# Performance work log

Measured on AMD Instinct MI355X. Metric: run time of the kernel, lower is better.

Reference implementation:

```python
import jax, jax.numpy as jnp
import numpy as np

B = 4096
D = 68 * 68  # 4624
L = 68
E = 1024


def setup_inputs() -> dict:
    key = jax.random.key(0)
    ks = jax.random.split(key, 24)
    rn = lambda k, shape, scale: jax.random.normal(k, shape, dtype=jnp.float32) * scale
    inp = {
        "x": rn(ks[0], (B, D), 1.0),
        "eps": rn(ks[1], (B, L), 1.0),
        # weights scaled ~1/sqrt(fan_in) to avoid sigmoid saturation
        "fc11_w": rn(ks[2], (E, D), 1.0 / np.sqrt(D)),
        "fc11_b": rn(ks[3], (E,), 0.01),
        "fc12_w": rn(ks[4], (E, D), 1.0 / np.sqrt(D)),
        "fc12_b": rn(ks[5], (E,), 0.01),
        "fc21_w": rn(ks[6], (L, E), 1.0 / np.sqrt(E)),
        "fc21_b": rn(ks[7], (L,), 0.01),
        "fc22_w": rn(ks[8], (L, E), 1.0 / np.sqrt(E)),
        "fc22_b": rn(ks[9], (L,), 0.01),
        "W3": rn(ks[10], (5, L, L), 1.0 / np.sqrt(L)),
        "b3": rn(ks[11], (5, L), 0.01),
        "W4": rn(ks[12], (5, L, L), 1.0 / np.sqrt(L)),
        "b4": rn(ks[13], (5, L), 0.01),
        "W5": rn(ks[14], (3, L, L), 1.0 / np.sqrt(L)),
        "b5": rn(ks[15], (3, L), 0.01),
        "fc6_w": rn(ks[16], (D, D), 1.0 / np.sqrt(D)),
        "fc6_b": rn(ks[17], (D,), 0.01),
        "fcy_w": rn(ks[18], (1, L), 1.0 / np.sqrt(L)),
        "fcy_b": rn(ks[19], (1,), 0.01),
    }
    return inp


def _forward(x, eps, fc11_w, fc11_b, fc12_w, fc12_b, fc21_w, fc21_b,
             fc22_w, fc22_b, W3, b3, W4, b4, W5, b5, fc6_w, fc6_b, fcy_w, fcy_b):
    b = x.shape[0]
    # encode (dropout in eval mode -> identity)
    h11 = jax.nn.relu(x @ fc11_w.T + fc11_b)
    h12 = jax.nn.relu(x @ fc12_w.T + fc12_b)
    mu = h11 @ fc21_w.T + fc21_b          # [B, 68]
    logvar = h12 @ fc22_w.T + fc22_b      # [B, 68]
    # reparameterize
    z = mu + eps * jnp.exp(0.5 * logvar)
    y = mu @ fcy_w.T + fcy_b              # [B, 1]
    # decode: 5 parallel 68-dim branches (vectorized over branch axis k)
    h3 = jnp.einsum('bd,kod->kbo', z, W3) + b3[:, None, :]     # [5,B,68]
    # source: h31 has no sigmoid, h32..h35 do
    h3 = jnp.concatenate([h3[:1], jax.nn.sigmoid(h3[1:])], axis=0)
    h4 = jax.nn.sigmoid(jnp.einsum('kbd,kod->kbo', h3, W4) + b4[:, None, :])
    # source reuses fc53 for branches 4 and 5: weight index map [0,1,2,2,2]
    idx = jnp.array([0, 1, 2, 2, 2])
    h5 = jnp.einsum('kbd,kod->kbo', h4, W5[idx]) + b5[idx][:, None, :]  # [5,B,68]
    # source: h6 = h51 only (other branch outer-products are dead code)
    h51 = h5[0]                                                # [B,68]
    outer = (h51[:, :, None] * h51[:, None, :]).reshape(b, D)  # bmm outer product
    recon = jax.nn.sigmoid(outer @ fc6_w.T + fc6_b)            # [B, 4624]
    return recon, mu, logvar, y


def reference(x, eps, fc11_w, fc11_b, fc12_w, fc12_b, fc21_w, fc21_b,
              fc22_w, fc22_b, W3, b3, W4, b4, W5, b5, fc6_w, fc6_b, fcy_w, fcy_b):
    return _forward(x, eps, fc11_w, fc11_b, fc12_w, fc12_b, fc21_w, fc21_b,
                    fc22_w, fc22_b, W3, b3, W4, b4, W5, b5, fc6_w, fc6_b, fcy_w, fcy_b)
```

## Files before the change

### kernel.cpp

```cpp
#include <hip/hip_runtime.h>
#include <hip/hip_bf16.h>
#include <cstdint>
#include <cstddef>

typedef __bf16 bf16x8 __attribute__((ext_vector_type(8)));
typedef __bf16 bf16x4 __attribute__((ext_vector_type(4)));
typedef float  floatx4 __attribute__((ext_vector_type(4)));

#define DEV __device__ __forceinline__

DEV __bf16 f2b(float x) { return (__bf16)x; }

DEV void async_ld16(const void* g, void* l) {
    __builtin_amdgcn_global_load_lds(
        (const __attribute__((address_space(1))) unsigned int*)g,
        (__attribute__((address_space(3))) unsigned int*)l,
        16, 0, 0);
}

#define BATCH 4096
#define DDIM  4624
#define DPAD  4800
#define LDIM  68
#define EDIM  1024
#define N1    2048
#define KB    2048
#define N2PAD 4864
#define NPAIR 2346
#define K2PAD 2496

__global__ void cvt_pad(const float* __restrict__ src, int rows_valid, int K,
                        __bf16* __restrict__ dst, int rows_total) {
    const int gpr = DPAD / 4;
    const long total = (long)rows_total * gpr;
    for (long g = blockIdx.x * (long)blockDim.x + threadIdx.x; g < total;
         g += gridDim.x * (long)blockDim.x) {
        int row = (int)(g / gpr);
        int c4  = (int)(g - (long)row * gpr) * 4;
        bf16x4 v;
        if (row < rows_valid && c4 < K) {
            floatx4 f = *(const floatx4*)(src + (size_t)row * K + c4);
            v[0] = f2b(f[0]); v[1] = f2b(f[1]); v[2] = f2b(f[2]); v[3] = f2b(f[3]);
        } else {
            v[0] = v[1] = v[2] = v[3] = (__bf16)0.0f;
        }
        *(bf16x4*)(dst + (size_t)row * DPAD + c4) = v;
    }
}

__global__ void pad_w2(const float* __restrict__ w21, const float* __restrict__ w22,
                       __bf16* __restrict__ dst) {
    const int total = 144 * 512;
    for (int g = blockIdx.x * blockDim.x + threadIdx.x; g < total;
         g += gridDim.x * blockDim.x) {
        int row = g >> 9;
        int c4  = (g & 511) * 4;
        bf16x4 v;
        v[0] = v[1] = v[2] = v[3] = (__bf16)0.0f;
        if (row < 68 && c4 < 1024) {
            floatx4 f = *(const floatx4*)(w21 + (size_t)row * EDIM + c4);
            v[0] = f2b(f[0]); v[1] = f2b(f[1]); v[2] = f2b(f[2]); v[3] = f2b(f[3]);
        } else if (row >= 68 && row < 136 && c4 >= 1024) {
            floatx4 f = *(const floatx4*)(w22 + (size_t)(row - 68) * EDIM + (c4 - 1024));
            v[0] = f2b(f[0]); v[1] = f2b(f[1]); v[2] = f2b(f[2]); v[3] = f2b(f[3]);
        }
        *(bf16x4*)(dst + (size_t)row * KB + c4) = v;
    }
}

DEV void build_ptab(unsigned short* ptab, int t, int nthr) {
    for (int i = t; i < LDIM; i += nthr) {
        int p0 = i * (137 - i) / 2;
        for (int j = i; j < LDIM; ++j)
            ptab[p0 + (j - i)] = (unsigned short)((i << 8) | j);
    }
}

__global__ void w6sym_build(const float* __restrict__ w6, __bf16* __restrict__ dst) {
    __shared__ float row[DDIM];
    __shared__ unsigned short ptab[K2PAD];
    const int o = blockIdx.x;
    const int t = threadIdx.x;
    if (o < DDIM) {
        const float* src = w6 + (size_t)o * DDIM;
        for (int idx = t; idx < DDIM / 4; idx += 256)
            *(floatx4*)(row + idx * 4) = *(const floatx4*)(src + idx * 4);
    }
    build_ptab(ptab, t, 256);
    __syncthreads();
    for (int p4 = t; p4 < K2PAD / 4; p4 += 256) {
        bf16x4 v;
#pragma unroll
        for (int u = 0; u < 4; ++u) {
            int p = p4 * 4 + u;
            float val = 0.f;
            if (o < DDIM && p < NPAIR) {
                int ij = ptab[p];
                int i = ij >> 8, j = ij & 255;
                val = (i == j) ? row[i * LDIM + i] : (row[i * LDIM + j] + row[j * LDIM + i]);
            }
            v[u] = f2b(val);
        }
        *(bf16x4*)(dst + (size_t)o * K2PAD + p4 * 4) = v;
    }
}

template <int EPI>
__launch_bounds__(512, 1)
__global__ void gemm_bt(const __bf16* __restrict__ A, int lda,
                        const __bf16* __restrict__ W, int ldb, int KT,
                        __bf16* __restrict__ outb, float* __restrict__ outf, int ldc,
                        const float* __restrict__ bias0, const float* __restrict__ bias1) {
    __shared__ __align__(16) __bf16 smA[3 * 128 * 64];
    __shared__ __align__(16) __bf16 smB[3 * 256 * 64];

    const int t  = threadIdx.x;
    const int l  = t & 63;
    const int w  = t >> 6;
    const int m0 = blockIdx.x * 128;
    const int n0 = blockIdx.y * 256;
    const int wm = (w & 1) * 64;
    const int wn = (w >> 1) * 64;

    const int lr = t >> 3;
    const int sw = (t & 7) ^ (lr & 7);
    const __bf16* pa0 = A + (size_t)(m0 + lr) * lda + sw * 8;
    const __bf16* pb0 = W + (size_t)(n0 + lr) * ldb + sw * 8;
    char* dA = (char*)smA + t * 16;
    char* dB = (char*)smB + t * 16;

    const int q  = l >> 4;
    const int ra = wm + (l & 15);
    const int rb = wn + (l & 15);

    floatx4 acc[4][4];
#pragma unroll
    for (int mi = 0; mi < 4; ++mi)
#pragma unroll
        for (int ni = 0; ni < 4; ++ni) {
            floatx4 z = {0.f, 0.f, 0.f, 0.f};
            acc[mi][ni] = z;
        }

    auto STAGE = [&](int tile, int buf) {
        const __bf16* sa = pa0 + (size_t)tile * 64;
        const __bf16* sb = pb0 + (size_t)tile * 64;
        char* da = dA + buf * 16384;
        char* db = dB + buf * 32768;
        async_ld16(sa,                        da);
        async_ld16(sa + (size_t)64  * lda,    da + 8192);
        async_ld16(sb,                        db);
        async_ld16(sb + (size_t)64  * ldb,    db + 8192);
        async_ld16(sb + (size_t)128 * ldb,    db + 16384);
        async_ld16(sb + (size_t)192 * ldb,    db + 24576);
    };

    auto COMPUTE = [&](int ba, int bb) {
        const char* baseA = (const char*)smA + ba;
        const char* baseB = (const char*)smB + bb;
#pragma unroll
        for (int h = 0; h < 2; ++h) {
            const int c = ((h << 2) | q) ^ (l & 7);
            bf16x8 af[4], bfr[4];
#pragma unroll
            for (int mi = 0; mi < 4; ++mi)
                af[mi] = *(const bf16x8*)(baseA + (ra + mi * 16) * 128 + c * 16);
#pragma unroll
            for (int ni = 0; ni < 4; ++ni)
                bfr[ni] = *(const bf16x8*)(baseB + (rb + ni * 16) * 128 + c * 16);
            __builtin_amdgcn_s_setprio(1);
#pragma unroll
            for (int mi = 0; mi < 4; ++mi)
#pragma unroll
                for (int ni = 0; ni < 4; ++ni)
                    acc[mi][ni] = __builtin_amdgcn_mfma_f32_16x16x32_bf16(
                        af[mi], bfr[ni], acc[mi][ni], 0, 0, 0);
            __builtin_amdgcn_s_setprio(0);
        }
    };

#define GBODY(BA, BB, DOSTG, STGT, STGBUF, VMS)                         \
    {                                                                   \
        asm volatile("s_waitcnt vmcnt(" VMS ")" ::: "memory");          \
        __builtin_amdgcn_s_barrier();                                   \
        __builtin_amdgcn_sched_barrier(0);                              \
        if (DOSTG) STAGE(STGT, STGBUF);                                 \
        COMPUTE(BA, BB);                                                \
    }

    STAGE(0, 0);
    STAGE(1, 1);

    int kt = 0;
    for (; kt < KT - 3; kt += 3) {
        GBODY(0,     0,     true, kt + 2, 2, "6");
        GBODY(16384, 32768, true, kt + 3, 0, "6");
        GBODY(32768, 65536, true, kt + 4, 1, "6");
    }
    GBODY(0,     0,     true,  kt + 2, 2, "6");
    GBODY(16384, 32768, false, 0,      0, "6");
    GBODY(32768, 65536, false, 0,      0, "0");
#undef GBODY

    const int colbase = n0 + wn + (l & 15);
    const int rowbase = m0 + wm + (l >> 4) * 4;
#pragma unroll
    for (int ni = 0; ni < 4; ++ni) {
        int col = colbase + ni * 16;
        if (EPI == 1 && col >= DDIM) continue;
        float bias = (EPI == 0)
                         ? ((col < 1024) ? bias0[col] : bias1[col - 1024])
                         : bias0[col];
#pragma unroll
        for (int mi = 0; mi < 4; ++mi) {
            int row = rowbase + mi * 16;
#pragma unroll
            for (int r = 0; r < 4; ++r) {
                float v = acc[mi][ni][r] + bias;
                if (EPI == 0) {
                    v = v > 0.f ? v : 0.f;
                    outb[(size_t)(row + r) * ldc + col] = f2b(v);
                } else {
                    v = 1.f / (1.f + __expf(-v));
                    outf[(size_t)(row + r) * ldc + col] = v;
                }
            }
        }
    }
}

__launch_bounds__(64, 4)
__global__ void gemmB(const __bf16* __restrict__ h, const __bf16* __restrict__ w2,
                      float* __restrict__ muvar) {
    const int l    = threadIdx.x;
    const int m0   = blockIdx.x * 16;
    const int k0   = blockIdx.y * 512;
    const int row  = l & 15;
    const int quad = l >> 4;

    floatx4 acc[9];
#pragma unroll
    for (int ni = 0; ni < 9; ++ni) {
        floatx4 z = {0.f, 0.f, 0.f, 0.f};
        acc[ni] = z;
    }

    const __bf16* ap = h + (size_t)(m0 + row) * KB + k0 + quad * 8;
    for (int kt = 0; kt < 16; ++kt) {
        bf16x8 a = *(const bf16x8*)ap;
        ap += 32;
#pragma unroll
        for (int ni = 0; ni < 9; ++ni) {
            const __bf16* bp = w2 + (size_t)(ni * 16 + row) * KB + k0 + kt * 32 + quad * 8;
            bf16x8 b = *(const bf16x8*)bp;
            acc[ni] = __builtin_amdgcn_mfma_f32_16x16x32_bf16(a, b, acc[ni], 0, 0, 0);
        }
    }
#pragma unroll
    for (int ni = 0; ni < 9; ++ni) {
        int col = ni * 16 + row;
        if (col < 136) {
#pragma unroll
            for (int r = 0; r < 4; ++r) {
                int orow = m0 + quad * 4 + r;
                atomicAdd(&muvar[(size_t)orow * 136 + col], acc[ni][r]);
            }
        }
    }
}

__global__ void decode(const float* __restrict__ muvar, const float* __restrict__ eps,
                       const float* __restrict__ b21, const float* __restrict__ b22,
                       const float* __restrict__ W3, const float* __restrict__ b3,
                       const float* __restrict__ W4, const float* __restrict__ b4,
                       const float* __restrict__ W5, const float* __restrict__ b5,
                       const float* __restrict__ fcyw, const float* __restrict__ fcyb,
                       float* __restrict__ out_mu, float* __restrict__ out_lv,
                       float* __restrict__ out_y, __bf16* __restrict__ A2) {
    __shared__ float w3s[DDIM], w4s[DDIM], w5s[DDIM];
    __shared__ float b3s[LDIM], b4s[LDIM], b5s[LDIM], fys[LDIM];
    __shared__ float zb[16][LDIM], h3b[16][LDIM], h51b[16][LDIM];
    __shared__ unsigned short ptab[K2PAD];

    const int t  = threadIdx.x;
    const int r0 = blockIdx.x * 16;

    for (int i = t; i < DDIM; i += 256) {
        w3s[i] = W3[i];
        w4s[i] = W4[i];
        w5s[i] = W5[i];
    }
    if (t < LDIM) {
        b3s[t] = b3[t];
        b4s[t] = b4[t];
        b5s[t] = b5[t];
        fys[t] = fcyw[t];
    }
    build_ptab(ptab, t, 256);
    __syncthreads();

    for (int idx = t; idx < 16 * LDIM; idx += 256) {
        int r = idx / LDIM, o = idx - r * LDIM;
        int row = r0 + r;
        float mu = muvar[(size_t)row * 136 + o] + b21[o];
        float lv = muvar[(size_t)row * 136 + 68 + o] + b22[o];
        float z  = mu + eps[(size_t)row * LDIM + o] * __expf(0.5f * lv);
        zb[r][o] = z;
        out_mu[(size_t)row * LDIM + o] = mu;
        out_lv[(size_t)row * LDIM + o] = lv;
    }
    if (t < 16) {
        int row = r0 + t;
        float s = fcyb[0];
        for (int o = 0; o < LDIM; ++o)
            s += (muvar[(size_t)row * 136 + o] + b21[o]) * fys[o];
        out_y[row] = s;
    }
    __syncthreads();

    for (int idx = t; idx < 16 * LDIM; idx += 256) {
        int r = idx / LDIM, o = idx - r * LDIM;
        float s = b3s[o];
        for (int d = 0; d < LDIM; ++d) s += zb[r][d] * w3s[o * LDIM + d];
        h3b[r][o] = s;
    }
    __syncthreads();

    for (int idx = t; idx < 16 * LDIM; idx += 256) {
        int r = idx / LDIM, o = idx - r * LDIM;
        float s = b4s[o];
        for (int d = 0; d < LDIM; ++d) s += h3b[r][d] * w4s[o * LDIM + d];
        zb[r][o] = 1.f / (1.f + __expf(-s));
    }
    __syncthreads();

    for (int idx = t; idx < 16 * LDIM; idx += 256) {
        int r = idx / LDIM, o = idx - r * LDIM;
        float s = b5s[o];
        for (int d = 0; d < LDIM; ++d) s += zb[r][d] * w5s[o * LDIM + d];
        h51b[r][o] = s;
    }
    __syncthreads();

    for (int idx = t; idx < 16 * (K2PAD / 4); idx += 256) {
        int r  = idx / (K2PAD / 4);
        int p4 = (idx - r * (K2PAD / 4)) * 4;
        int row = r0 + r;
        bf16x4 v;
#pragma unroll
        for (int u = 0; u < 4; ++u) {
            int p = p4 + u;
            float val = 0.f;
            if (p < NPAIR) {
                int ij = ptab[p];
                val = h51b[r][ij >> 8] * h51b[r][ij & 255];
            }
            v[u] = f2b(val);
        }
        *(bf16x4*)(A2 + (size_t)row * K2PAD + p4) = v;
    }
}

extern "C" void kernel_launch(void* const* d_in, const int* in_sizes, int n_in,
                              void* d_out, int out_size, void* d_ws, size_t ws_size,
                              hipStream_t stream) {
    const float* x    = (const float*)d_in[0];
    const float* eps  = (const float*)d_in[1];
    const float* w11  = (const float*)d_in[2];
    const float* b11  = (const float*)d_in[3];
    const float* w12  = (const float*)d_in[4];
    const float* b12  = (const float*)d_in[5];
    const float* w21  = (const float*)d_in[6];
    const float* b21  = (const float*)d_in[7];
    const float* w22  = (const float*)d_in[8];
    const float* b22  = (const float*)d_in[9];
    const float* W3   = (const float*)d_in[10];
    const float* b3   = (const float*)d_in[11];
    const float* W4   = (const float*)d_in[12];
    const float* b4   = (const float*)d_in[13];
    const float* W5   = (const float*)d_in[14];
    const float* b5   = (const float*)d_in[15];
    const float* w6   = (const float*)d_in[16];
    const float* b6   = (const float*)d_in[17];
    const float* fcyw = (const float*)d_in[18];
    const float* fcyb = (const float*)d_in[19];

    float* out       = (float*)d_out;
    float* out_recon = out;
    float* out_mu    = out + (size_t)BATCH * DDIM;
    float* out_lv    = out_mu + (size_t)BATCH * LDIM;
    float* out_y     = out_lv + (size_t)BATCH * LDIM;

    char* ws = (char*)d_ws;
    size_t off = 0;
    __bf16* xb     = (__bf16*)(ws + off); off += (size_t)BATCH * DPAD * 2;
    __bf16* w1_pad = (__bf16*)(ws + off); off += (size_t)N1 * DPAD * 2;
    __bf16* w6s    = (__bf16*)(ws + off); off += (size_t)N2PAD * K2PAD * 2;
    __bf16* hbuf   = (__bf16*)(ws + off); off += (size_t)BATCH * KB * 2;
    __bf16* w2_pad = (__bf16*)(ws + off); off += (size_t)144 * KB * 2;
    float*  muvar  = (float*) (ws + off); off += (size_t)BATCH * 136 * 4;
    __bf16* A2     = (__bf16*)(ws + off);

    hipMemsetAsync(muvar, 0, (size_t)BATCH * 136 * 4, stream);

    cvt_pad<<<2048, 256, 0, stream>>>(x, BATCH, DDIM, xb, BATCH);
    cvt_pad<<<512, 256, 0, stream>>>(w11, 1024, DDIM, w1_pad, 1024);
    cvt_pad<<<512, 256, 0, stream>>>(w12, 1024, DDIM, w1_pad + (size_t)1024 * DPAD, 1024);
    w6sym_build<<<N2PAD, 256, 0, stream>>>(w6, w6s);
    pad_w2<<<72, 256, 0, stream>>>(w21, w22, w2_pad);

    gemm_bt<0><<<dim3(BATCH / 128, N1 / 256), 512, 0, stream>>>(
        xb, DPAD, w1_pad, DPAD, DPAD / 64, hbuf, nullptr, N1, b11, b12);

    gemmB<<<dim3(BATCH / 16, 4), 64, 0, stream>>>(hbuf, w2_pad, muvar);

    decode<<<BATCH / 16, 256, 0, stream>>>(muvar, eps, b21, b22, W3, b3, W4, b4, W5, b5,
                                           fcyw, fcyb, out_mu, out_lv, out_y, A2);

    gemm_bt<1><<<dim3(BATCH / 128, N2PAD / 256), 512, 0, stream>>>(
        A2, K2PAD, w6s, K2PAD, K2PAD / 64, nullptr, out_recon, DDIM, b6, nullptr);
}
```

Baseline: 560.5 us.

## Split GEMM k-tile into two half-steps interleaving async staging with MFMA

```diff
diff --git a/kernel.cpp b/kernel.cpp
--- a/kernel.cpp
+++ b/kernel.cpp
@@ -129,9 +129,11 @@
     char* dA = (char*)smA + t * 16;
     char* dB = (char*)smB + t * 16;
 
-    const int q  = l >> 4;
-    const int ra = wm + (l & 15);
-    const int rb = wn + (l & 15);
+    const int q   = l >> 4;
+    const int ra  = wm + (l & 15);
+    const int rb  = wn + (l & 15);
+    const int c0b = ((0 | q) ^ (l & 7)) * 16;
+    const int c1b = ((4 | q) ^ (l & 7)) * 16;
 
     floatx4 acc[4][4];
 #pragma unroll
@@ -142,65 +144,82 @@
             acc[mi][ni] = z;
         }
 
-    auto STAGE = [&](int tile, int buf) {
+    auto STG0 = [&](int tile, int ba, int bb) {
         const __bf16* sa = pa0 + (size_t)tile * 64;
         const __bf16* sb = pb0 + (size_t)tile * 64;
-        char* da = dA + buf * 16384;
-        char* db = dB + buf * 32768;
-        async_ld16(sa,                        da);
-        async_ld16(sa + (size_t)64  * lda,    da + 8192);
-        async_ld16(sb,                        db);
-        async_ld16(sb + (size_t)64  * ldb,    db + 8192);
-        async_ld16(sb + (size_t)128 * ldb,    db + 16384);
-        async_ld16(sb + (size_t)192 * ldb,    db + 24576);
+        async_ld16(sa,                      dA + ba);
+        async_ld16(sa + (size_t)64 * lda,   dA + ba + 8192);
+        async_ld16(sb,                      dB + bb);
     };
-
-    auto COMPUTE = [&](int ba, int bb) {
-        const char* baseA = (const char*)smA + ba;
-        const char* baseB = (const char*)smB + bb;
-#pragma unroll
-        for (int h = 0; h < 2; ++h) {
-            const int c = ((h << 2) | q) ^ (l & 7);
-            bf16x8 af[4], bfr[4];
-#pragma unroll
-            for (int mi = 0; mi < 4; ++mi)
-                af[mi] = *(const bf16x8*)(baseA + (ra + mi * 16) * 128 + c * 16);
+    auto STG1 = [&](int tile, int bb) {
+        const __bf16* sb = pb0 + (size_t)tile * 64;
+        async_ld16(sb + (size_t)64 * ldb,   dB + bb + 8192);
+        async_ld16(sb + (size_t)128 * ldb,  dB + bb + 16384);
+        async_ld16(sb + (size_t)192 * ldb,  dB + bb + 24576);
+    };
+    auto LOADFRAGS = [&](const char* baA, const char* baB, int cb,
+                         bf16x8* af, bf16x8* bfr) {
+#pragma unroll
+        for (int mi = 0; mi < 4; ++mi)
+            af[mi] = *(const bf16x8*)(baA + (ra + mi * 16) * 128 + cb);
+#pragma unroll
+        for (int ni = 0; ni < 4; ++ni)
+            bfr[ni] = *(const bf16x8*)(baB + (rb + ni * 16) * 128 + cb);
+    };
+    auto MFMA16 = [&](bf16x8* af, bf16x8* bfr) {
+        __builtin_amdgcn_s_setprio(1);
+#pragma unroll
+        for (int mi = 0; mi < 4; ++mi)
 #pragma unroll
             for (int ni = 0; ni < 4; ++ni)
-                bfr[ni] = *(const bf16x8*)(baseB + (rb + ni * 16) * 128 + c * 16);
-            __builtin_amdgcn_s_setprio(1);
-#pragma unroll
-            for (int mi = 0; mi < 4; ++mi)
-#pragma unroll
-                for (int ni = 0; ni < 4; ++ni)
-                    acc[mi][ni] = __builtin_amdgcn_mfma_f32_16x16x32_bf16(
-                        af[mi], bfr[ni], acc[mi][ni], 0, 0, 0);
-            __builtin_amdgcn_s_setprio(0);
-        }
+                acc[mi][ni] = __builtin_amdgcn_mfma_f32_16x16x32_bf16(
+                    af[mi], bfr[ni], acc[mi][ni], 0, 0, 0);
+        __builtin_amdgcn_s_setprio(0);
     };
 
-#define GBODY(BA, BB, DOSTG, STGT, STGBUF, VMS)                         \
-    {                                                                   \
-        asm volatile("s_waitcnt vmcnt(" VMS ")" ::: "memory");          \
-        __builtin_amdgcn_s_barrier();                                   \
-        __builtin_amdgcn_sched_barrier(0);                              \
-        if (DOSTG) STAGE(STGT, STGBUF);                                 \
-        COMPUTE(BA, BB);                                                \
-    }
-
-    STAGE(0, 0);
-    STAGE(1, 1);
-
-    int kt = 0;
-    for (; kt < KT - 3; kt += 3) {
-        GBODY(0,     0,     true, kt + 2, 2, "6");
-        GBODY(16384, 32768, true, kt + 3, 0, "6");
-        GBODY(32768, 65536, true, kt + 4, 1, "6");
-    }
-    GBODY(0,     0,     true,  kt + 2, 2, "6");
-    GBODY(16384, 32768, false, 0,      0, "6");
-    GBODY(32768, 65536, false, 0,      0, "0");
-#undef GBODY
+#define TILE(BA, BB, SEN, ST, SBA, SBB, EVM)                                \
+    {                                                                       \
+        const char* baA = (const char*)smA + (BA);                          \
+        const char* baB = (const char*)smB + (BB);                          \
+        bf16x8 af[4], bfr[4];                                               \
+                                                     \
+        LOADFRAGS(baA, baB, c0b, af, bfr);                                  \
+        if (SEN) STG0(ST, SBA, SBB);                                        \
+        __builtin_amdgcn_s_barrier();                                       \
+        asm volatile("s_waitcnt lgkmcnt(0)" ::: "memory");                  \
+        __builtin_amdgcn_sched_barrier(0);                                  \
+        MFMA16(af, bfr);                                                    \
+        __builtin_amdgcn_s_barrier();                                       \
+                                                     \
+        LOADFRAGS(baA, baB, c1b, af, bfr);                                  \
+        if (SEN) STG1(ST, SBB);                                             \
+        __builtin_amdgcn_s_barrier();                                       \
+        asm volatile("s_waitcnt lgkmcnt(0)" ::: "memory");                  \
+        __builtin_amdgcn_sched_barrier(0);                                  \
+        MFMA16(af, bfr);                                                    \
+        if (EVM == 6) asm volatile("s_waitcnt vmcnt(6)" ::: "memory");      \
+        else if (EVM == 0) asm volatile("s_waitcnt vmcnt(0)" ::: "memory"); \
+        __builtin_amdgcn_s_barrier();                                       \
+    }
+
+    enum { A1 = 16384, A2O = 32768, B1 = 32768, B2O = 65536 };
+
+    STG0(0, 0, 0);   STG1(0, 0);
+    STG0(1, A1, B1); STG1(1, B1);
+    asm volatile("s_waitcnt vmcnt(6)" ::: "memory");
+    __builtin_amdgcn_s_barrier();
+
+    const int G = KT / 3;
+    for (int g = 0; g < G - 1; ++g) {
+        const int tt = g * 3;
+        TILE(0,   0,   1, tt + 2, A2O, B2O, 6);
+        TILE(A1,  B1,  1, tt + 3, 0,   0,   6);
+        TILE(A2O, B2O, 1, tt + 4, A1,  B1,  6);
+    }
+    TILE(0,   0,   1, KT - 1, A2O, B2O, 6);
+    TILE(A1,  B1,  0, 0, 0, 0, 0);
+    TILE(A2O, B2O, 0, 0, 0, 0, -1);
+#undef TILE
 
     const int colbase = n0 + wn + (l & 15);
     const int rowbase = m0 + wm + (l >> 4) * 4;
```

Measured after the change: 567.9 us. Within noise of the previous version (+1.3%).
